# Performance work log

Measured on AMD Instinct MI355X. Metric: run time of the kernel, lower is better.

## Reference

```python
import jax, jax.numpy as jnp
import numpy as np

N, T, F, H = 4096, 365, 16, 32
N_CLASSES = 1
STD = 0.02


def setup_inputs() -> dict:
    key = jax.random.key(0)
    ks = jax.random.split(key, 16)
    rn = lambda k, shp: jax.random.normal(k, shp, dtype=jnp.float32) * STD
    return {
        "x": jax.random.normal(ks[0], (N, T, F), dtype=jnp.float32),
        "A": jax.random.uniform(ks[1], (N, N), dtype=jnp.float32),
        "W_out": rn(ks[2], (H, N_CLASSES)),
        "b_out": jnp.zeros((N_CLASSES,), jnp.float32),
        "W_graph_h": rn(ks[3], (H, H)),
        "b_graph_h": jnp.zeros((H,), jnp.float32),
        "W_graph_c": rn(ks[4], (H, H)),
        "b_graph_c": jnp.zeros((H,), jnp.float32),
        "W_h_cur": rn(ks[5], (H, H)),
        "W_h_prev": rn(ks[6], (H, H)),
        "b_h": jnp.zeros((H,), jnp.float32),
        "W_c_cur": rn(ks[7], (H, H)),
        "W_c_prev": rn(ks[8], (H, H)),
        "b_c": jnp.zeros((H,), jnp.float32),
        "lstm_kernel": rn(ks[9], (F, 4 * H)),
        "lstm_rec": rn(ks[10], (H, 4 * H)),
        "lstm_bias": jnp.zeros((4 * H,), jnp.float32),
    }


def reference(x, A, W_out, b_out, W_graph_h, b_graph_h, W_graph_c, b_graph_c,
              W_h_cur, W_h_prev, b_h, W_c_cur, W_c_prev, b_c,
              lstm_kernel, lstm_rec, lstm_bias):
    n, t, f = x.shape
    h = W_out.shape[0]
    x_t = jnp.swapaxes(x, 0, 1)  # [T, N, F]

    def step(carry, xt):
        h_prev, c_prev = carry
        # graph message passing on previous hidden/cell states
        h_graph = jnp.tanh(A @ (h_prev @ W_graph_h + b_graph_h))
        c_graph = jnp.tanh(A @ (c_prev @ W_graph_c + b_graph_c))
        # standard LSTM cell (i, f, g, o gate order as in tf.keras.layers.LSTMCell)
        gates = xt @ lstm_kernel + h_prev @ lstm_rec + lstm_bias
        i_g, f_g, g_g, o_g = jnp.split(gates, 4, axis=-1)
        c_cur = jax.nn.sigmoid(f_g) * c_prev + jax.nn.sigmoid(i_g) * jnp.tanh(g_g)
        h_cur = jax.nn.sigmoid(o_g) * jnp.tanh(c_cur)
        # fuse LSTM state with graph-propagated state
        h_upd = jax.nn.sigmoid(h_cur @ W_h_cur + h_graph @ W_h_prev + b_h)
        c_upd = jax.nn.sigmoid(c_cur @ W_c_cur + c_graph @ W_c_prev + b_c)
        return (h_upd, c_upd), h_upd

    init = (jnp.zeros((n, h), x.dtype), jnp.zeros((n, h), x.dtype))
    _, outs = jax.lax.scan(step, init, x_t)  # [T, N, H]
    out = outs.reshape(-1, h)  # [T*N, H], matches tf.reshape of time-major list
    return out @ W_out + b_out  # [T*N, 1]
```

## Files before the change

kernel.cpp:

```cpp
#include <hip/hip_runtime.h>
#include <math.h>

#define NN 4096
#define TT 365
#define FF 16
#define HH 32

typedef _Float16 f16;
typedef __attribute__((ext_vector_type(8))) _Float16 f16x8;
typedef __attribute__((ext_vector_type(4))) float f32x4;

__device__ __forceinline__ float sigf(float x){ return 1.0f/(1.0f+__expf(-x)); }
__device__ __forceinline__ float thf(float x){
    x = fminf(fmaxf(x,-15.0f),15.0f);
    float e = __expf(2.0f*x);
    return (e-1.0f)/(e+1.0f);
}

__global__ __launch_bounds__(256)
void prep_A(const float* __restrict__ A, f16* __restrict__ Af){
    size_t i = (size_t)blockIdx.x*256 + threadIdx.x;
    int lane = (int)(i & 63);
    int kt   = (int)((i>>6) & 127);
    int rb   = (int)(i>>13);
    int m  = rb*16 + (lane&15);
    int k0 = kt*32 + ((lane>>4)<<3);
    const float* src = A + (size_t)m*NN + k0;
    float4 a = *(const float4*)src;
    float4 b = *(const float4*)(src+4);
    float v[8] = {a.x,a.y,a.z,a.w,b.x,b.y,b.z,b.w};
    f16x8 vh;
    #pragma unroll
    for (int j=0;j<8;++j) vh[j] = (f16)v[j];
    ((f16x8*)Af)[i] = vh;
}

__global__ __launch_bounds__(256)
void init_G(f16* __restrict__ G, float* __restrict__ hs, float* __restrict__ cs,
            const float* __restrict__ bgh, const float* __restrict__ bgc){
    int i = blockIdx.x*256 + threadIdx.x;
    int k = i>>6, n = i&63;
    float v = (n<HH) ? bgh[n] : bgc[n-HH];
    int kt = k>>5, kr = k&31;
    size_t idx = (((size_t)kt*4 + (n>>4))*64 + ((n&15) + ((kr>>3)<<4)))*8 + (kr&7);
    G[idx] = (f16)v;
    if (i < NN*HH){ hs[i]=0.f; cs[i]=0.f; }
}

__global__ __launch_bounds__(256, 6)
void mm_kernel(const f16* __restrict__ Af, const f16* __restrict__ Gin,
               float* __restrict__ Pbuf)
{
    __shared__ float red[4096];
    const int tid  = threadIdx.x;
    const int w    = tid >> 6;
    const int lane = tid & 63;
    const int pair = blockIdx.x >> 3;
    const int kq   = blockIdx.x & 7;
    const int band0 = pair*2, band1 = pair*2 + 1;
    const int ktBeg = kq*16 + w*4;

    const f16x8* Ahp = (const f16x8*)Af;
    const f16x8* Gf  = (const f16x8*)Gin;
    size_t a0 = ((size_t)band0*128 + ktBeg)*64 + lane;
    size_t a1 = ((size_t)band1*128 + ktBeg)*64 + lane;
    size_t g  = (size_t)ktBeg*256 + lane;

    f32x4 acc0[4] = {}, acc1[4] = {};
    #pragma unroll
    for (int kt = 0; kt < 4; ++kt, a0 += 64, a1 += 64, g += 256){
        f16x8 A0 = Ahp[a0], A1 = Ahp[a1];
        f16x8 g0 = Gf[g], g1 = Gf[g+64], g2 = Gf[g+128], g3 = Gf[g+192];
        acc0[0] = __builtin_amdgcn_mfma_f32_16x16x32_f16(A0,g0,acc0[0],0,0,0);
        acc0[1] = __builtin_amdgcn_mfma_f32_16x16x32_f16(A0,g1,acc0[1],0,0,0);
        acc0[2] = __builtin_amdgcn_mfma_f32_16x16x32_f16(A0,g2,acc0[2],0,0,0);
        acc0[3] = __builtin_amdgcn_mfma_f32_16x16x32_f16(A0,g3,acc0[3],0,0,0);
        acc1[0] = __builtin_amdgcn_mfma_f32_16x16x32_f16(A1,g0,acc1[0],0,0,0);
        acc1[1] = __builtin_amdgcn_mfma_f32_16x16x32_f16(A1,g1,acc1[1],0,0,0);
        acc1[2] = __builtin_amdgcn_mfma_f32_16x16x32_f16(A1,g2,acc1[2],0,0,0);
        acc1[3] = __builtin_amdgcn_mfma_f32_16x16x32_f16(A1,g3,acc1[3],0,0,0);
    }
    const int mr = (lane>>4)<<2, mc = lane&15;
    if (w < 2){
        #pragma unroll
        for (int ct = 0; ct < 4; ++ct)
            #pragma unroll
            for (int r = 0; r < 4; ++r){
                red[w*2048 +        (mr+r)*64 + ct*16 + mc] = acc0[ct][r];
                red[w*2048 + 1024 + (mr+r)*64 + ct*16 + mc] = acc1[ct][r];
            }
    }
    __syncthreads();
    if (w >= 2){
        #pragma unroll
        for (int ct = 0; ct < 4; ++ct)
            #pragma unroll
            for (int r = 0; r < 4; ++r){
                red[(w-2)*2048 +        (mr+r)*64 + ct*16 + mc] += acc0[ct][r];
                red[(w-2)*2048 + 1024 + (mr+r)*64 + ct*16 + mc] += acc1[ct][r];
            }
    }
    __syncthreads();
    #pragma unroll
    for (int q = 0; q < 8; ++q){
        int e = tid + q*256;
        float s = red[e] + red[2048 + e];
        int bnd = e >> 10;
        Pbuf[(size_t)kq*262144 + (size_t)(band0 + bnd)*1024 + (e & 1023)] = s;
    }
}

__global__ __launch_bounds__(512)
void cell_kernel(const float* __restrict__ Pbuf,
                 const float* __restrict__ x, const float* __restrict__ W_out,
                 const float* __restrict__ b_out,
                 const float* __restrict__ Wgh, const float* __restrict__ bgh,
                 const float* __restrict__ Wgc, const float* __restrict__ bgc,
                 const float* __restrict__ Whc, const float* __restrict__ Whp,
                 const float* __restrict__ bh,
                 const float* __restrict__ Wcc, const float* __restrict__ Wcp,
                 const float* __restrict__ bc,
                 const float* __restrict__ K, const float* __restrict__ R,
                 const float* __restrict__ bias,
                 f16* __restrict__ Gout,
                 float* __restrict__ h_state, float* __restrict__ c_state,
                 float* __restrict__ out, int t)
{
    __shared__ float smem[6000];
    float* gts    = smem;
    float* hgcg   = smem + 2064;
    float* hprevL = smem + 3104;
    float* xs     = smem + 3632;
    float* hcur   = smem + 3888;
    float* ccur   = smem + 4416;
    float* hupd   = smem + 4944;
    float* cupd   = smem + 5472;

    const int tid = threadIdx.x;
    const int r2  = tid >> 5;
    const int j   = tid & 31;
    const int band = blockIdx.x;
    const int row = band*16 + r2;

    #pragma unroll
    for (int half = 0; half < 2; ++half){
        int n = j + half*32;
        float s = 0.f;
        #pragma unroll
        for (int q = 0; q < 8; ++q)
            s += Pbuf[(size_t)q*262144 + (size_t)band*1024 + r2*64 + n];
        hgcg[r2*65 + n] = thf(s);
    }

    float hp = h_state[(size_t)row*HH + j];
    hprevL[r2*33 + j] = hp;
    if (j < 16) xs[r2*16 + j] = x[((size_t)row*TT + t)*FF + j];

    float g4[4];
    #pragma unroll
    for (int q = 0; q < 4; ++q) g4[q] = bias[j*4 + q];
    #pragma unroll
    for (int f = 0; f < FF; ++f){
        float xv = xs[r2*16 + f];
        float4 k4 = *(const float4*)(K + f*128 + j*4);
        g4[0] += xv*k4.x; g4[1] += xv*k4.y; g4[2] += xv*k4.z; g4[3] += xv*k4.w;
    }
    #pragma unroll
    for (int i = 0; i < HH; ++i){
        float hv = hprevL[r2*33 + i];
        float4 r4 = *(const float4*)(R + i*128 + j*4);
        g4[0] += hv*r4.x; g4[1] += hv*r4.y; g4[2] += hv*r4.z; g4[3] += hv*r4.w;
    }
    #pragma unroll
    for (int q = 0; q < 4; ++q) gts[r2*129 + j*4 + q] = g4[q];

    float gi = gts[r2*129 + j],      gf = gts[r2*129 + 32 + j];
    float gg = gts[r2*129 + 64 + j], go = gts[r2*129 + 96 + j];
    float cp = c_state[(size_t)row*HH + j];
    float cc = sigf(gf)*cp + sigf(gi)*thf(gg);
    float hc = sigf(go)*thf(cc);
    hcur[r2*33 + j] = hc;
    ccur[r2*33 + j] = cc;

    float s = bh[j], u = bc[j];
    #pragma unroll
    for (int i = 0; i < HH; ++i){
        float hcv = hcur[r2*33 + i], hgv = hgcg[r2*65 + i];
        float ccv = ccur[r2*33 + i], cgv = hgcg[r2*65 + 32 + i];
        s += hcv*Whc[i*32 + j] + hgv*Whp[i*32 + j];
        u += ccv*Wcc[i*32 + j] + cgv*Wcp[i*32 + j];
    }
    float hu = sigf(s), cu = sigf(u);
    hupd[r2*33 + j] = hu;
    cupd[r2*33 + j] = cu;
    h_state[(size_t)row*HH + j] = hu;
    c_state[(size_t)row*HH + j] = cu;

    float gh = bgh[j], gc = bgc[j];
    #pragma unroll
    for (int i = 0; i < HH; ++i){
        float hv = hupd[r2*33 + i], cv = cupd[r2*33 + i];
        gh += hv*Wgh[i*32 + j];
        gc += cv*Wgc[i*32 + j];
    }
    {
        const int kt = row>>5, kr = row&31;
        const size_t tb = ((size_t)kt*4)*64;
        size_t i0 = (tb + (size_t)(j>>4)*64 + ((j&15) + ((kr>>3)<<4)))*8 + (kr&7);
        size_t i1 = (tb + (size_t)((HH+j)>>4)*64 + ((j&15) + ((kr>>3)<<4)))*8 + (kr&7);
        Gout[i0] = (f16)gh;
        Gout[i1] = (f16)gc;
    }

    float p = hu * W_out[j];
    #pragma unroll
    for (int off = 16; off; off >>= 1) p += __shfl_down(p, off, 32);
    if (j == 0) out[(size_t)t*NN + row] = p + b_out[0];
}

extern "C" void kernel_launch(void* const* d_in, const int* in_sizes, int n_in,
                              void* d_out, int out_size, void* d_ws, size_t ws_size,
                              hipStream_t stream)
{
    const float* x     = (const float*)d_in[0];
    const float* A     = (const float*)d_in[1];
    const float* W_out = (const float*)d_in[2];
    const float* b_out = (const float*)d_in[3];
    const float* Wgh   = (const float*)d_in[4];
    const float* bgh   = (const float*)d_in[5];
    const float* Wgc   = (const float*)d_in[6];
    const float* bgc   = (const float*)d_in[7];
    const float* Whc   = (const float*)d_in[8];
    const float* Whp   = (const float*)d_in[9];
    const float* bh    = (const float*)d_in[10];
    const float* Wcc   = (const float*)d_in[11];
    const float* Wcp   = (const float*)d_in[12];
    const float* bc    = (const float*)d_in[13];
    const float* K     = (const float*)d_in[14];
    const float* R     = (const float*)d_in[15];
    const float* bias  = (const float*)d_in[16];
    float* out = (float*)d_out;

    f16* Af = (f16*)d_ws;
    f16* G0 = Af + (size_t)NN*NN;
    f16* G1 = G0 + (size_t)NN*64;
    float* Pbuf = (float*)(G1 + (size_t)NN*64);
    float* hs = Pbuf + (size_t)8*NN*64;
    float* cs = hs + (size_t)NN*HH;

    prep_A<<<dim3(8192), dim3(256), 0, stream>>>(A, Af);
    init_G<<<dim3(1024), dim3(256), 0, stream>>>(G0, hs, cs, bgh, bgc);

    for (int t = 0; t < TT; ++t){
        const f16* Gin = (t & 1) ? G1 : G0;
        f16*       Gout = (t & 1) ? G0 : G1;
        mm_kernel<<<dim3(1024), dim3(256), 0, stream>>>(Af, Gin, Pbuf);
        cell_kernel<<<dim3(256), dim3(512), 0, stream>>>(
            Pbuf, x, W_out, b_out, Wgh, bgh, Wgc, bgc, Whc, Whp, bh,
            Wcc, Wcp, bc, K, R, bias, Gout, hs, cs, out, t);
    }
}
```

Baseline: 6.673 ms.

## Switch A@G matmul to 32x32x16 MFMA tiles with 4-way K split

Reworks the per-step A@G matmul to use 32x32x16 MFMA instructions, with 512-thread blocks covering 32 rows and a quarter of K each. A and G are re-packed into matching fragment layouts, and the split-K partial buffer goes from 8 slices to 4, so the cell kernel reads fewer partials. Shared-memory reduction grows to 64KB per block, which may limit occupancy, and each wave now holds larger accumulators.

```diff
diff --git a/kernel.cpp b/kernel.cpp
--- a/kernel.cpp
+++ b/kernel.cpp
@@ -8,7 +8,7 @@
 
 typedef _Float16 f16;
 typedef __attribute__((ext_vector_type(8))) _Float16 f16x8;
-typedef __attribute__((ext_vector_type(4))) float f32x4;
+typedef __attribute__((ext_vector_type(16))) float f32x16;
 
 __device__ __forceinline__ float sigf(float x){ return 1.0f/(1.0f+__expf(-x)); }
 __device__ __forceinline__ float thf(float x){
@@ -21,10 +21,10 @@
 void prep_A(const float* __restrict__ A, f16* __restrict__ Af){
     size_t i = (size_t)blockIdx.x*256 + threadIdx.x;
     int lane = (int)(i & 63);
-    int kt   = (int)((i>>6) & 127);
-    int rb   = (int)(i>>13);
-    int m  = rb*16 + (lane&15);
-    int k0 = kt*32 + ((lane>>4)<<3);
+    int kc   = (int)((i>>6) & 255);
+    int rg   = (int)(i>>14);
+    int m  = rg*32 + (lane&31);
+    int k0 = kc*16 + ((lane>>5)<<3);
     const float* src = A + (size_t)m*NN + k0;
     float4 a = *(const float4*)src;
     float4 b = *(const float4*)(src+4);
@@ -41,72 +41,66 @@
     int i = blockIdx.x*256 + threadIdx.x;
     int k = i>>6, n = i&63;
     float v = (n<HH) ? bgh[n] : bgc[n-HH];
-    int kt = k>>5, kr = k&31;
-    size_t idx = (((size_t)kt*4 + (n>>4))*64 + ((n&15) + ((kr>>3)<<4)))*8 + (kr&7);
+    size_t idx = (((size_t)(k>>4)*2 + (n>>5))*64 + ((n&31) + (((k>>3)&1)<<5)))*8 + (k&7);
     G[idx] = (f16)v;
     if (i < NN*HH){ hs[i]=0.f; cs[i]=0.f; }
 }
 
-__global__ __launch_bounds__(256, 6)
+__global__ __launch_bounds__(512, 4)
 void mm_kernel(const f16* __restrict__ Af, const f16* __restrict__ Gin,
                float* __restrict__ Pbuf)
 {
-    __shared__ float red[4096];
+    __shared__ float red[16384];
     const int tid  = threadIdx.x;
     const int w    = tid >> 6;
     const int lane = tid & 63;
-    const int pair = blockIdx.x >> 3;
-    const int kq   = blockIdx.x & 7;
-    const int band0 = pair*2, band1 = pair*2 + 1;
-    const int ktBeg = kq*16 + w*4;
-
+    const int rg   = blockIdx.x >> 2;
+    const int kq   = blockIdx.x & 3;
+
+    const int kcBeg = kq*64 + w*8;
     const f16x8* Ahp = (const f16x8*)Af;
     const f16x8* Gf  = (const f16x8*)Gin;
-    size_t a0 = ((size_t)band0*128 + ktBeg)*64 + lane;
-    size_t a1 = ((size_t)band1*128 + ktBeg)*64 + lane;
-    size_t g  = (size_t)ktBeg*256 + lane;
-
-    f32x4 acc0[4] = {}, acc1[4] = {};
-    #pragma unroll
-    for (int kt = 0; kt < 4; ++kt, a0 += 64, a1 += 64, g += 256){
-        f16x8 A0 = Ahp[a0], A1 = Ahp[a1];
-        f16x8 g0 = Gf[g], g1 = Gf[g+64], g2 = Gf[g+128], g3 = Gf[g+192];
-        acc0[0] = __builtin_amdgcn_mfma_f32_16x16x32_f16(A0,g0,acc0[0],0,0,0);
-        acc0[1] = __builtin_amdgcn_mfma_f32_16x16x32_f16(A0,g1,acc0[1],0,0,0);
-        acc0[2] = __builtin_amdgcn_mfma_f32_16x16x32_f16(A0,g2,acc0[2],0,0,0);
-        acc0[3] = __builtin_amdgcn_mfma_f32_16x16x32_f16(A0,g3,acc0[3],0,0,0);
-        acc1[0] = __builtin_amdgcn_mfma_f32_16x16x32_f16(A1,g0,acc1[0],0,0,0);
-        acc1[1] = __builtin_amdgcn_mfma_f32_16x16x32_f16(A1,g1,acc1[1],0,0,0);
-        acc1[2] = __builtin_amdgcn_mfma_f32_16x16x32_f16(A1,g2,acc1[2],0,0,0);
-        acc1[3] = __builtin_amdgcn_mfma_f32_16x16x32_f16(A1,g3,acc1[3],0,0,0);
-    }
-    const int mr = (lane>>4)<<2, mc = lane&15;
-    if (w < 2){
+    size_t aIdx = ((size_t)rg*256 + kcBeg)*64 + lane;
+    size_t gIdx = ((size_t)kcBeg*2)*64 + lane;
+
+    f32x16 acc0 = {}, acc1 = {};
+    #pragma unroll
+    for (int kc = 0; kc < 8; ++kc, aIdx += 64, gIdx += 128){
+        f16x8 a0 = Ahp[aIdx];
+        f16x8 g0 = Gf[gIdx], g1 = Gf[gIdx+64];
+        acc0 = __builtin_amdgcn_mfma_f32_32x32x16_f16(a0, g0, acc0, 0,0,0);
+        acc1 = __builtin_amdgcn_mfma_f32_32x32x16_f16(a0, g1, acc1, 0,0,0);
+    }
+    const int c0 = lane & 31;
+    const int rbase = (lane>>5)<<2;
+    if (w < 4){
         #pragma unroll
-        for (int ct = 0; ct < 4; ++ct)
-            #pragma unroll
-            for (int r = 0; r < 4; ++r){
-                red[w*2048 +        (mr+r)*64 + ct*16 + mc] = acc0[ct][r];
-                red[w*2048 + 1024 + (mr+r)*64 + ct*16 + mc] = acc1[ct][r];
-            }
+        for (int reg = 0; reg < 16; ++reg){
+            int r = (reg&3) + ((reg>>2)<<3) + rbase;
+            red[(w<<11) + r*64 + c0]      = acc0[reg];
+            red[(w<<11) + r*64 + 32 + c0] = acc1[reg];
+        }
     }
     __syncthreads();
-    if (w >= 2){
+    if (w >= 4){
         #pragma unroll
-        for (int ct = 0; ct < 4; ++ct)
-            #pragma unroll
-            for (int r = 0; r < 4; ++r){
-                red[(w-2)*2048 +        (mr+r)*64 + ct*16 + mc] += acc0[ct][r];
-                red[(w-2)*2048 + 1024 + (mr+r)*64 + ct*16 + mc] += acc1[ct][r];
-            }
+        for (int reg = 0; reg < 16; ++reg){
+            int r = (reg&3) + ((reg>>2)<<3) + rbase;
+            red[((w-4)<<11) + r*64 + c0]      += acc0[reg];
+            red[((w-4)<<11) + r*64 + 32 + c0] += acc1[reg];
+        }
     }
     __syncthreads();
-    #pragma unroll
-    for (int q = 0; q < 8; ++q){
-        int e = tid + q*256;
-        float s = red[e] + red[2048 + e];
-        int bnd = e >> 10;
-        Pbuf[(size_t)kq*262144 + (size_t)(band0 + bnd)*1024 + (e & 1023)] = s;
+    {
+        int e = tid*4;
+        float4 s0 = *(const float4*)(red + e);
+        float4 s1 = *(const float4*)(red + 2048 + e);
+        float4 s2 = *(const float4*)(red + 4096 + e);
+        float4 s3 = *(const float4*)(red + 6144 + e);
+        float4 s;
+        s.x = s0.x+s1.x+s2.x+s3.x; s.y = s0.y+s1.y+s2.y+s3.y;
+        s.z = s0.z+s1.z+s2.z+s3.z; s.w = s0.w+s1.w+s2.w+s3.w;
+        *(float4*)(Pbuf + ((size_t)kq*128 + rg)*2048 + e) = s;
     }
 }
 
@@ -141,14 +135,16 @@
     const int j   = tid & 31;
     const int band = blockIdx.x;
     const int row = band*16 + r2;
+    const int rg  = band >> 1;
+    const int rIn = (band & 1)*16 + r2;
 
     #pragma unroll
     for (int half = 0; half < 2; ++half){
         int n = j + half*32;
         float s = 0.f;
         #pragma unroll
-        for (int q = 0; q < 8; ++q)
-            s += Pbuf[(size_t)q*262144 + (size_t)band*1024 + r2*64 + n];
+        for (int q = 0; q < 4; ++q)
+            s += Pbuf[((size_t)q*128 + rg)*2048 + rIn*64 + n];
         hgcg[r2*65 + n] = thf(s);
     }
 
@@ -204,10 +200,11 @@
         gc += cv*Wgc[i*32 + j];
     }
     {
-        const int kt = row>>5, kr = row&31;
-        const size_t tb = ((size_t)kt*4)*64;
-        size_t i0 = (tb + (size_t)(j>>4)*64 + ((j&15) + ((kr>>3)<<4)))*8 + (kr&7);
-        size_t i1 = (tb + (size_t)((HH+j)>>4)*64 + ((j&15) + ((kr>>3)<<4)))*8 + (kr&7);
+        const int kc = row>>4;
+        const int kb = ((row>>3)&1)<<5;
+        const int kj = row&7;
+        size_t i0 = (((size_t)kc*2 + 0)*64 + (j + kb))*8 + kj;
+        size_t i1 = (((size_t)kc*2 + 1)*64 + (j + kb))*8 + kj;
         Gout[i0] = (f16)gh;
         Gout[i1] = (f16)gc;
     }
@@ -245,7 +242,7 @@
     f16* G0 = Af + (size_t)NN*NN;
     f16* G1 = G0 + (size_t)NN*64;
     float* Pbuf = (float*)(G1 + (size_t)NN*64);
-    float* hs = Pbuf + (size_t)8*NN*64;
+    float* hs = Pbuf + (size_t)4*128*2048;
     float* cs = hs + (size_t)NN*HH;
 
     prep_A<<<dim3(8192), dim3(256), 0, stream>>>(A, Af);
@@ -254,7 +251,7 @@
     for (int t = 0; t < TT; ++t){
         const f16* Gin = (t & 1) ? G1 : G0;
         f16*       Gout = (t & 1) ? G0 : G1;
-        mm_kernel<<<dim3(1024), dim3(256), 0, stream>>>(Af, Gin, Pbuf);
+        mm_kernel<<<dim3(512), dim3(512), 0, stream>>>(Af, Gin, Pbuf);
         cell_kernel<<<dim3(256), dim3(512), 0, stream>>>(
             Pbuf, x, W_out, b_out, Wgh, bgh, Wgc, bgc, Whc, Whp, bh,
             Wcc, Wcp, bc, K, R, bias, Gout, hs, cs, out, t);
```

Measured after the change: 6.938 ms. +4.0%, slower.
